# Kernel optimization log

Hardware: AMD Instinct MI355X
Metric: run time of the kernel (lower is better)

## Reference

```python
import jax, jax.numpy as jnp
import numpy as np

B, I, H = 4096, 1024, 1024

def setup_inputs() -> dict:
    key = jax.random.key(0)
    ks = jax.random.split(key, 10)
    return {
        "input": jax.random.normal(ks[0], (B, I), dtype=jnp.float32),
        "hx": jax.random.normal(ks[1], (B, H), dtype=jnp.float32),
        "cx": jax.random.normal(ks[2], (B, H), dtype=jnp.float32),
        "noise_q": jax.random.uniform(ks[3], (1,), dtype=jnp.float32),
        "noise_e": jax.random.uniform(ks[4], (1,), dtype=jnp.float32),
        "weight_ih": jax.random.normal(ks[5], (4 * H, I), dtype=jnp.float32),
        "weight_hh": jax.random.normal(ks[6], (4 * H, H), dtype=jnp.float32),
        "bias_ih": jax.random.normal(ks[7], (4 * H,), dtype=jnp.float32),
        "bias_hh": jax.random.normal(ks[8], (4 * H,), dtype=jnp.float32),
        # pre-drawn standard-normal noise (torch.randn in the original forward)
        "eps_c": jax.random.normal(jax.random.fold_in(key, 101), (B, H), dtype=jnp.float32),
        "eps_h": jax.random.normal(jax.random.fold_in(key, 102), (B, H), dtype=jnp.float32),
    }

def reference(input, hx, cx, noise_q, noise_e, weight_ih, weight_hh, bias_ih, bias_hh, eps_c, eps_h):
    # gates: [B, 4H]
    gates = input @ weight_ih.T + bias_ih + hx @ weight_hh.T + bias_hh
    ingate, forgetgate, cellgate, outgate = jnp.split(gates, 4, axis=1)
    ingate = jax.nn.sigmoid(ingate)
    forgetgate = jax.nn.sigmoid(forgetgate)
    cellgate = jnp.tanh(cellgate)
    outgate = jax.nn.sigmoid(outgate)
    cy = forgetgate * cx + ingate * cellgate + jnp.sqrt(noise_e) * eps_c
    hy = outgate * jnp.tanh(cy) + jnp.sqrt(noise_q) * eps_h
    return (hy, cy)
```

## Files before the change

kernel.cpp:

```cpp
#include <hip/hip_runtime.h>
#include <hip/hip_bf16.h>
#include <cstdint>
#include <cstddef>


#define B_ROWS 4096
#define HDIM   1024
#define KDIM   2048
#define BM     256
#define BK     32
#define T_STEPS (KDIM / BK)

typedef unsigned short u16;
using f32x4  = __attribute__((ext_vector_type(4))) float;
using short8 = __attribute__((ext_vector_type(8))) short;
using half8  = __attribute__((ext_vector_type(8))) _Float16;

__device__ __forceinline__ u16 f2h_bits(float f) {
    _Float16 h = (_Float16)f;
    return __builtin_bit_cast(u16, h);
}

__global__ void pack_kernel(const float* __restrict__ input, const float* __restrict__ hx,
                            const float* __restrict__ wih, const float* __restrict__ whh,
                            u16* __restrict__ Af, u16* __restrict__ Wf)
{
    const int PER = (B_ROWS * KDIM) / 4;
    int stride = gridDim.x * blockDim.x;
    for (int i = blockIdx.x * blockDim.x + threadIdx.x; i < 2 * PER; i += stride) {
        int isW = (i >= PER) ? 1 : 0;
        int e = i - isW * PER;
        int row = e >> 9;
        int k = (e & 511) << 2;
        const float* s0 = isW ? wih : input;
        const float* s1 = isW ? whh : hx;
        const float* src = (k < 1024) ? (s0 + (size_t)row * 1024 + k)
                                      : (s1 + (size_t)row * 1024 + (k - 1024));
        float4 v = *(const float4*)src;
        size_t doff = (size_t)row * KDIM + k;
        u16* dst = (isW ? Wf : Af) + doff;
        *(ushort4*)dst = make_ushort4(f2h_bits(v.x), f2h_bits(v.y),
                                      f2h_bits(v.z), f2h_bits(v.w));
    }
}

__device__ __forceinline__ void gload16(const void* g, void* l) {
    __builtin_amdgcn_global_load_lds((const __attribute__((address_space(1))) void*)g,
                                     (__attribute__((address_space(3))) void*)l, 16, 0, 0);
}
__device__ __forceinline__ float sigmf(float x) { return 1.0f / (1.0f + __expf(-x)); }
__device__ __forceinline__ float tanhfast(float x) { return 1.0f - 2.0f / (1.0f + __expf(2.0f * x)); }

__launch_bounds__(512, 2)
__global__ void lstm_fused(const u16* __restrict__ Afp, const u16* __restrict__ Wfp,
                           const float* __restrict__ cx, const float* __restrict__ eps_c,
                           const float* __restrict__ eps_h,
                           const float* __restrict__ bias_ih, const float* __restrict__ bias_hh,
                           const float* __restrict__ noise_q, const float* __restrict__ noise_e,
                           float* __restrict__ out)
{
    __shared__ __align__(16) u16 lA[3][4][256][8];
    __shared__ __align__(16) u16 lW[3][4][256][8];

    int bid = blockIdx.x;
    int w = (bid & 7) * 32 + (bid >> 3);
    int mi = w & 15;
    int hq = w >> 4;
    int bm0 = mi * BM;
    int h0 = hq * 64;

    int tid  = threadIdx.x;
    int lane = tid & 63;
    int wid  = tid >> 6;
    int wm   = wid >> 2;
    int wn   = wid & 3;

    int rSt = tid & 255;
    int kS  = tid >> 8;
    const u16* Asrc = Afp + (size_t)(bm0 + rSt) * KDIM;
    int wgrow = (rSt >> 6) * 1024 + h0 + (rSt & 63);
    const u16* Wsrc = Wfp + (size_t)wgrow * KDIM;

#define STG_A(sb, t_) do { \
        gload16(Asrc + (t_) * 32 + kS * 8,       &lA[sb][kS][rSt][0]);     \
        gload16(Asrc + (t_) * 32 + (kS + 2) * 8, &lA[sb][kS + 2][rSt][0]); } while (0)
#define STG_W(sb, t_) do { \
        gload16(Wsrc + (t_) * 32 + kS * 8,       &lW[sb][kS][rSt][0]);     \
        gload16(Wsrc + (t_) * 32 + (kS + 2) * 8, &lW[sb][kS + 2][rSt][0]); } while (0)

    int fk = lane >> 4, fr = lane & 15;

    f32x4 acc[8][4];
#pragma unroll
    for (int m = 0; m < 8; ++m)
#pragma unroll
        for (int g = 0; g < 4; ++g)
            acc[m][g] = (f32x4){0.f, 0.f, 0.f, 0.f};

    STG_A(0, 0); STG_W(0, 0);
    STG_A(1, 1); STG_W(1, 1);
    asm volatile("s_waitcnt vmcnt(4)");
    __builtin_amdgcn_s_barrier();

#define LD8(p) __builtin_bit_cast(half8, *(const short8*)(p))

#define PH_MFMA(mb, A0, A1, A2, A3) do { \
        __builtin_amdgcn_s_setprio(1); \
        _Pragma("unroll") \
        for (int g = 0; g < 4; ++g) { \
            acc[(mb)][g]     = __builtin_amdgcn_mfma_f32_16x16x32_f16(A0, wf[g], acc[(mb)][g], 0, 0, 0); \
            acc[(mb) + 1][g] = __builtin_amdgcn_mfma_f32_16x16x32_f16(A1, wf[g], acc[(mb) + 1][g], 0, 0, 0); \
        } \
        _Pragma("unroll") \
        for (int g = 0; g < 4; ++g) { \
            acc[(mb) + 2][g] = __builtin_amdgcn_mfma_f32_16x16x32_f16(A2, wf[g], acc[(mb) + 2][g], 0, 0, 0); \
            acc[(mb) + 3][g] = __builtin_amdgcn_mfma_f32_16x16x32_f16(A3, wf[g], acc[(mb) + 3][g], 0, 0, 0); \
        } \
        __builtin_amdgcn_s_setprio(0); \
    } while (0)

#define WAIT_LGKM() do { \
        asm volatile("s_waitcnt lgkmcnt(0)"); \
        __builtin_amdgcn_sched_barrier(0); \
    } while (0)

#pragma unroll 1
    for (int t = 0; t < T_STEPS; ++t) {
        int scur = t % 3;
        int spre = (t + 2) % 3;
        bool pre = (t < T_STEPS - 2);
        const u16* pA = &lA[scur][fk][wm * 128 + fr][0];
        const u16* pW = &lW[scur][fk][wn * 16 + fr][0];

        half8 wf[4];
        half8 a0, a1, a2, a3, b0, b1, b2, b3;

#pragma unroll
        for (int g = 0; g < 4; ++g) wf[g] = LD8(pW + g * 512);
        a0 = LD8(pA);           a1 = LD8(pA + 128);
        a2 = LD8(pA + 2 * 128); a3 = LD8(pA + 3 * 128);
        if (pre) STG_A(spre, t + 2);
        __builtin_amdgcn_s_barrier();
        WAIT_LGKM();
        PH_MFMA(0, a0, a1, a2, a3);
        __builtin_amdgcn_s_barrier();

        b0 = LD8(pA + 4 * 128); b1 = LD8(pA + 5 * 128);
        b2 = LD8(pA + 6 * 128); b3 = LD8(pA + 7 * 128);
        if (pre) STG_W(spre, t + 2);
        __builtin_amdgcn_s_barrier();
        WAIT_LGKM();
        PH_MFMA(4, b0, b1, b2, b3);
        if (pre) asm volatile("s_waitcnt vmcnt(4)");
        else     asm volatile("s_waitcnt vmcnt(0)");
        __builtin_amdgcn_s_barrier();
        __builtin_amdgcn_sched_barrier(0);
    }

    float sq_e = sqrtf(noise_e[0]);
    float sq_q = sqrtf(noise_q[0]);
    int h = h0 + wn * 16 + fr;
    float bsum[4];
#pragma unroll
    for (int g = 0; g < 4; ++g)
        bsum[g] = bias_ih[g * 1024 + h] + bias_hh[g * 1024 + h];
#pragma unroll
    for (int m = 0; m < 8; ++m) {
        int r0 = bm0 + wm * 128 + m * 16 + fk * 4;
#pragma unroll
        for (int j = 0; j < 4; ++j) {
            int r = r0 + j;
            float gi = acc[m][0][j] + bsum[0];
            float gf = acc[m][1][j] + bsum[1];
            float gc = acc[m][2][j] + bsum[2];
            float go = acc[m][3][j] + bsum[3];
            float ig = sigmf(gi), fg = sigmf(gf);
            float cg = tanhfast(gc), og = sigmf(go);
            size_t off = (size_t)r * HDIM + h;
            float cyv = fg * cx[off] + ig * cg + sq_e * eps_c[off];
            float hyv = og * tanhfast(cyv) + sq_q * eps_h[off];
            out[off] = hyv;
            out[(size_t)B_ROWS * HDIM + off] = cyv;
        }
    }
}

extern "C" void kernel_launch(void* const* d_in, const int* in_sizes, int n_in,
                              void* d_out, int out_size, void* d_ws, size_t ws_size,
                              hipStream_t stream)
{
    const float* input = (const float*)d_in[0];
    const float* hx    = (const float*)d_in[1];
    const float* cx    = (const float*)d_in[2];
    const float* nq    = (const float*)d_in[3];
    const float* ne    = (const float*)d_in[4];
    const float* wih   = (const float*)d_in[5];
    const float* whh   = (const float*)d_in[6];
    const float* bih   = (const float*)d_in[7];
    const float* bhh   = (const float*)d_in[8];
    const float* epsc  = (const float*)d_in[9];
    const float* epsh  = (const float*)d_in[10];
    float* out = (float*)d_out;

    u16* Af = (u16*)d_ws;
    u16* Wf = Af + (size_t)B_ROWS * KDIM;

    hipLaunchKernelGGL(pack_kernel, dim3(2048), dim3(256), 0, stream,
                       input, hx, wih, whh, Af, Wf);
    hipLaunchKernelGGL(lstm_fused, dim3(256), dim3(512), 0, stream,
                       Af, Wf, cx, epsc, epsh, bih, bhh, nq, ne, out);
}
```

Before: 113.4 us.

## Double the K tile and switch to double-buffered LDS pipeline

Raises BK from 32 to 64 and replaces the triple-buffered, two-tiles-ahead prefetch with a double buffer that prefetches one tile ahead, issuing all next-tile loads at the top of each iteration. Each iteration now runs twice as many MFMAs per barrier pair, which halves loop iterations and barrier overhead. The cost is a shallower prefetch, so global latency may be less hidden because the loop waits for vmcnt(0) every iteration. LDS use rises from 96KB to 128KB per block, which may affect occupancy at 2 blocks per CU.

```diff
diff --git a/kernel.cpp b/kernel.cpp
--- a/kernel.cpp
+++ b/kernel.cpp
@@ -8,7 +8,7 @@
 #define HDIM   1024
 #define KDIM   2048
 #define BM     256
-#define BK     32
+#define BK     64
 #define T_STEPS (KDIM / BK)
 
 typedef unsigned short u16;
@@ -59,8 +59,8 @@
                            const float* __restrict__ noise_q, const float* __restrict__ noise_e,
                            float* __restrict__ out)
 {
-    __shared__ __align__(16) u16 lA[3][4][256][8];
-    __shared__ __align__(16) u16 lW[3][4][256][8];
+    __shared__ __align__(16) u16 lA[2][8][256][8];
+    __shared__ __align__(16) u16 lW[2][8][256][8];
 
     int bid = blockIdx.x;
     int w = (bid & 7) * 32 + (bid >> 3);
@@ -81,14 +81,22 @@
     int wgrow = (rSt >> 6) * 1024 + h0 + (rSt & 63);
     const u16* Wsrc = Wfp + (size_t)wgrow * KDIM;
 
-#define STG_A(sb, t_) do { \
-        gload16(Asrc + (t_) * 32 + kS * 8,       &lA[sb][kS][rSt][0]);     \
-        gload16(Asrc + (t_) * 32 + (kS + 2) * 8, &lA[sb][kS + 2][rSt][0]); } while (0)
-#define STG_W(sb, t_) do { \
-        gload16(Wsrc + (t_) * 32 + kS * 8,       &lW[sb][kS][rSt][0]);     \
-        gload16(Wsrc + (t_) * 32 + (kS + 2) * 8, &lW[sb][kS + 2][rSt][0]); } while (0)
+#define STG_A(b, t_) do { \
+        _Pragma("unroll") \
+        for (int s = 0; s < 4; ++s) { \
+            int kc = kS + 2 * s; \
+            gload16(Asrc + (t_) * 64 + kc * 8, &lA[b][kc][rSt][0]); \
+        } } while (0)
+#define STG_W(b, t_) do { \
+        _Pragma("unroll") \
+        for (int s = 0; s < 4; ++s) { \
+            int kc = kS + 2 * s; \
+            gload16(Wsrc + (t_) * 64 + kc * 8, &lW[b][kc][rSt][0]); \
+        } } while (0)
 
     int fk = lane >> 4, fr = lane & 15;
+    const u16* pAbase = &lA[0][0][0][0] + fk * 2048 + (wm * 128 + fr) * 8;
+    const u16* pWbase = &lW[0][0][0][0] + fk * 2048 + (wn * 16 + fr) * 8;
 
     f32x4 acc[8][4];
 #pragma unroll
@@ -98,25 +106,22 @@
             acc[m][g] = (f32x4){0.f, 0.f, 0.f, 0.f};
 
     STG_A(0, 0); STG_W(0, 0);
-    STG_A(1, 1); STG_W(1, 1);
-    asm volatile("s_waitcnt vmcnt(4)");
+    asm volatile("s_waitcnt vmcnt(0)");
     __builtin_amdgcn_s_barrier();
 
 #define LD8(p) __builtin_bit_cast(half8, *(const short8*)(p))
 
-#define PH_MFMA(mb, A0, A1, A2, A3) do { \
-        __builtin_amdgcn_s_setprio(1); \
+#define MFMA16(mb, A0, A1, A2, A3, WF) do { \
         _Pragma("unroll") \
         for (int g = 0; g < 4; ++g) { \
-            acc[(mb)][g]     = __builtin_amdgcn_mfma_f32_16x16x32_f16(A0, wf[g], acc[(mb)][g], 0, 0, 0); \
-            acc[(mb) + 1][g] = __builtin_amdgcn_mfma_f32_16x16x32_f16(A1, wf[g], acc[(mb) + 1][g], 0, 0, 0); \
+            acc[(mb)][g]     = __builtin_amdgcn_mfma_f32_16x16x32_f16(A0, WF[g], acc[(mb)][g], 0, 0, 0); \
+            acc[(mb) + 1][g] = __builtin_amdgcn_mfma_f32_16x16x32_f16(A1, WF[g], acc[(mb) + 1][g], 0, 0, 0); \
         } \
         _Pragma("unroll") \
         for (int g = 0; g < 4; ++g) { \
-            acc[(mb) + 2][g] = __builtin_amdgcn_mfma_f32_16x16x32_f16(A2, wf[g], acc[(mb) + 2][g], 0, 0, 0); \
-            acc[(mb) + 3][g] = __builtin_amdgcn_mfma_f32_16x16x32_f16(A3, wf[g], acc[(mb) + 3][g], 0, 0, 0); \
+            acc[(mb) + 2][g] = __builtin_amdgcn_mfma_f32_16x16x32_f16(A2, WF[g], acc[(mb) + 2][g], 0, 0, 0); \
+            acc[(mb) + 3][g] = __builtin_amdgcn_mfma_f32_16x16x32_f16(A3, WF[g], acc[(mb) + 3][g], 0, 0, 0); \
         } \
-        __builtin_amdgcn_s_setprio(0); \
     } while (0)
 
 #define WAIT_LGKM() do { \
@@ -126,33 +131,43 @@
 
 #pragma unroll 1
     for (int t = 0; t < T_STEPS; ++t) {
-        int scur = t % 3;
-        int spre = (t + 2) % 3;
-        bool pre = (t < T_STEPS - 2);
-        const u16* pA = &lA[scur][fk][wm * 128 + fr][0];
-        const u16* pW = &lW[scur][fk][wn * 16 + fr][0];
-
-        half8 wf[4];
+        const int cur = t & 1;
+        const bool pre = (t < T_STEPS - 1);
+        const u16* pA = pAbase + cur * 16384;
+        const u16* pW = pWbase + cur * 16384;
+
+        half8 wf0[4], wf1[4];
         half8 a0, a1, a2, a3, b0, b1, b2, b3;
 
-#pragma unroll
-        for (int g = 0; g < 4; ++g) wf[g] = LD8(pW + g * 512);
+        if (pre) { STG_A(cur ^ 1, t + 1); STG_W(cur ^ 1, t + 1); }
+#pragma unroll
+        for (int g = 0; g < 4; ++g) {
+            wf0[g] = LD8(pW + g * 512);
+            wf1[g] = LD8(pW + 8192 + g * 512);
+        }
         a0 = LD8(pA);           a1 = LD8(pA + 128);
-        a2 = LD8(pA + 2 * 128); a3 = LD8(pA + 3 * 128);
-        if (pre) STG_A(spre, t + 2);
+        a2 = LD8(pA + 256);     a3 = LD8(pA + 384);
+        b0 = LD8(pA + 8192);        b1 = LD8(pA + 8192 + 128);
+        b2 = LD8(pA + 8192 + 256);  b3 = LD8(pA + 8192 + 384);
         __builtin_amdgcn_s_barrier();
         WAIT_LGKM();
-        PH_MFMA(0, a0, a1, a2, a3);
-        __builtin_amdgcn_s_barrier();
-
-        b0 = LD8(pA + 4 * 128); b1 = LD8(pA + 5 * 128);
-        b2 = LD8(pA + 6 * 128); b3 = LD8(pA + 7 * 128);
-        if (pre) STG_W(spre, t + 2);
+        __builtin_amdgcn_s_setprio(1);
+        MFMA16(0, a0, a1, a2, a3, wf0);
+        MFMA16(0, b0, b1, b2, b3, wf1);
+        __builtin_amdgcn_s_setprio(0);
+        __builtin_amdgcn_s_barrier();
+
+        a0 = LD8(pA + 512);         a1 = LD8(pA + 640);
+        a2 = LD8(pA + 768);         a3 = LD8(pA + 896);
+        b0 = LD8(pA + 8192 + 512);  b1 = LD8(pA + 8192 + 640);
+        b2 = LD8(pA + 8192 + 768);  b3 = LD8(pA + 8192 + 896);
         __builtin_amdgcn_s_barrier();
         WAIT_LGKM();
-        PH_MFMA(4, b0, b1, b2, b3);
-        if (pre) asm volatile("s_waitcnt vmcnt(4)");
-        else     asm volatile("s_waitcnt vmcnt(0)");
+        __builtin_amdgcn_s_setprio(1);
+        MFMA16(4, a0, a1, a2, a3, wf0);
+        MFMA16(4, b0, b1, b2, b3, wf1);
+        __builtin_amdgcn_s_setprio(0);
+        asm volatile("s_waitcnt vmcnt(0)");
         __builtin_amdgcn_s_barrier();
         __builtin_amdgcn_sched_barrier(0);
     }
```

Result: slower. 155.6 us (+37.2%).

## Load weight fragments directly from global into registers, bypassing LDS staging

Applied to the files above, without the earlier changes.

The weight operand no longer goes through shared memory. Each wave now loads its own weight fragments straight from global memory into a register double buffer, one K-step ahead, while the activation tile is still staged through a triple-buffered LDS ring. The main loop is unrolled by two so the register buffers can alternate. This removes half of the LDS footprint and the LDS write/read traffic for weights. In exchange, the waves that share a column slice now issue duplicate, strided 16-byte global loads, and weight load latency is hidden by only one step of register prefetch.

```diff
diff --git a/kernel.cpp b/kernel.cpp
--- a/kernel.cpp
+++ b/kernel.cpp
@@ -60,7 +60,6 @@
                            float* __restrict__ out)
 {
     __shared__ __align__(16) u16 lA[3][4][256][8];
-    __shared__ __align__(16) u16 lW[3][4][256][8];
 
     int bid = blockIdx.x;
     int w = (bid & 7) * 32 + (bid >> 3);
@@ -78,17 +77,17 @@
     int rSt = tid & 255;
     int kS  = tid >> 8;
     const u16* Asrc = Afp + (size_t)(bm0 + rSt) * KDIM;
-    int wgrow = (rSt >> 6) * 1024 + h0 + (rSt & 63);
-    const u16* Wsrc = Wfp + (size_t)wgrow * KDIM;
 
 #define STG_A(sb, t_) do { \
         gload16(Asrc + (t_) * 32 + kS * 8,       &lA[sb][kS][rSt][0]);     \
         gload16(Asrc + (t_) * 32 + (kS + 2) * 8, &lA[sb][kS + 2][rSt][0]); } while (0)
-#define STG_W(sb, t_) do { \
-        gload16(Wsrc + (t_) * 32 + kS * 8,       &lW[sb][kS][rSt][0]);     \
-        gload16(Wsrc + (t_) * 32 + (kS + 2) * 8, &lW[sb][kS + 2][rSt][0]); } while (0)
 
     int fk = lane >> 4, fr = lane & 15;
+
+    const u16* WregB[4];
+#pragma unroll
+    for (int g = 0; g < 4; ++g)
+        WregB[g] = Wfp + (size_t)(g * 1024 + h0 + wn * 16 + fr) * KDIM + fk * 8;
 
     f32x4 acc[8][4];
 #pragma unroll
@@ -97,64 +96,66 @@
         for (int g = 0; g < 4; ++g)
             acc[m][g] = (f32x4){0.f, 0.f, 0.f, 0.f};
 
-    STG_A(0, 0); STG_W(0, 0);
-    STG_A(1, 1); STG_W(1, 1);
-    asm volatile("s_waitcnt vmcnt(4)");
+#define LD8(p) __builtin_bit_cast(half8, *(const short8*)(p))
+
+    half8 wfA[4], wfB[4];
+#pragma unroll
+    for (int g = 0; g < 4; ++g) wfA[g] = LD8(WregB[g]);
+    STG_A(0, 0);
+    STG_A(1, 1);
+    asm volatile("s_waitcnt vmcnt(2)");
     __builtin_amdgcn_s_barrier();
 
-#define LD8(p) __builtin_bit_cast(half8, *(const short8*)(p))
-
-#define PH_MFMA(mb, A0, A1, A2, A3) do { \
-        __builtin_amdgcn_s_setprio(1); \
+#define MFMA16(mb, A0, A1, A2, A3, WF) do { \
         _Pragma("unroll") \
         for (int g = 0; g < 4; ++g) { \
-            acc[(mb)][g]     = __builtin_amdgcn_mfma_f32_16x16x32_f16(A0, wf[g], acc[(mb)][g], 0, 0, 0); \
-            acc[(mb) + 1][g] = __builtin_amdgcn_mfma_f32_16x16x32_f16(A1, wf[g], acc[(mb) + 1][g], 0, 0, 0); \
+            acc[(mb)][g]     = __builtin_amdgcn_mfma_f32_16x16x32_f16(A0, WF[g], acc[(mb)][g], 0, 0, 0); \
+            acc[(mb) + 1][g] = __builtin_amdgcn_mfma_f32_16x16x32_f16(A1, WF[g], acc[(mb) + 1][g], 0, 0, 0); \
         } \
         _Pragma("unroll") \
         for (int g = 0; g < 4; ++g) { \
-            acc[(mb) + 2][g] = __builtin_amdgcn_mfma_f32_16x16x32_f16(A2, wf[g], acc[(mb) + 2][g], 0, 0, 0); \
-            acc[(mb) + 3][g] = __builtin_amdgcn_mfma_f32_16x16x32_f16(A3, wf[g], acc[(mb) + 3][g], 0, 0, 0); \
+            acc[(mb) + 2][g] = __builtin_amdgcn_mfma_f32_16x16x32_f16(A2, WF[g], acc[(mb) + 2][g], 0, 0, 0); \
+            acc[(mb) + 3][g] = __builtin_amdgcn_mfma_f32_16x16x32_f16(A3, WF[g], acc[(mb) + 3][g], 0, 0, 0); \
         } \
-        __builtin_amdgcn_s_setprio(0); \
     } while (0)
 
-#define WAIT_LGKM() do { \
+#define STEP(t_, WFU, WFL) do { \
+        const int scur = (t_) % 3; \
+        const int spre = ((t_) + 2) % 3; \
+        const u16* pA = &lA[scur][fk][wm * 128 + fr][0]; \
+        half8 a0, a1, a2, a3, a4, a5, a6, a7; \
+         \
+        if ((t_) < T_STEPS - 1) { \
+            _Pragma("unroll") \
+            for (int g = 0; g < 4; ++g) WFL[g] = LD8(WregB[g] + ((t_) + 1) * 32); \
+        } \
+        if ((t_) < T_STEPS - 2) STG_A(spre, (t_) + 2); \
+        a0 = LD8(pA);       a1 = LD8(pA + 128); \
+        a2 = LD8(pA + 256); a3 = LD8(pA + 384); \
+        __builtin_amdgcn_s_barrier(); \
         asm volatile("s_waitcnt lgkmcnt(0)"); \
         __builtin_amdgcn_sched_barrier(0); \
+        __builtin_amdgcn_s_setprio(1); \
+        MFMA16(0, a0, a1, a2, a3, WFU); \
+        __builtin_amdgcn_s_setprio(0); \
+        __builtin_amdgcn_s_barrier(); \
+         \
+        a4 = LD8(pA + 512); a5 = LD8(pA + 640); \
+        a6 = LD8(pA + 768); a7 = LD8(pA + 896); \
+        __builtin_amdgcn_s_barrier(); \
+        asm volatile("s_waitcnt lgkmcnt(0)"); \
+        __builtin_amdgcn_sched_barrier(0); \
+        __builtin_amdgcn_s_setprio(1); \
+        MFMA16(4, a4, a5, a6, a7, WFU); \
+        __builtin_amdgcn_s_setprio(0); \
+        asm volatile("s_waitcnt vmcnt(2)");   \
+        __builtin_amdgcn_s_barrier(); \
     } while (0)
 
 #pragma unroll 1
-    for (int t = 0; t < T_STEPS; ++t) {
-        int scur = t % 3;
-        int spre = (t + 2) % 3;
-        bool pre = (t < T_STEPS - 2);
-        const u16* pA = &lA[scur][fk][wm * 128 + fr][0];
-        const u16* pW = &lW[scur][fk][wn * 16 + fr][0];
-
-        half8 wf[4];
-        half8 a0, a1, a2, a3, b0, b1, b2, b3;
-
-#pragma unroll
-        for (int g = 0; g < 4; ++g) wf[g] = LD8(pW + g * 512);
-        a0 = LD8(pA);           a1 = LD8(pA + 128);
-        a2 = LD8(pA + 2 * 128); a3 = LD8(pA + 3 * 128);
-        if (pre) STG_A(spre, t + 2);
-        __builtin_amdgcn_s_barrier();
-        WAIT_LGKM();
-        PH_MFMA(0, a0, a1, a2, a3);
-        __builtin_amdgcn_s_barrier();
-
-        b0 = LD8(pA + 4 * 128); b1 = LD8(pA + 5 * 128);
-        b2 = LD8(pA + 6 * 128); b3 = LD8(pA + 7 * 128);
-        if (pre) STG_W(spre, t + 2);
-        __builtin_amdgcn_s_barrier();
-        WAIT_LGKM();
-        PH_MFMA(4, b0, b1, b2, b3);
-        if (pre) asm volatile("s_waitcnt vmcnt(4)");
-        else     asm volatile("s_waitcnt vmcnt(0)");
-        __builtin_amdgcn_s_barrier();
-        __builtin_amdgcn_sched_barrier(0);
+    for (int tt = 0; tt < T_STEPS; tt += 2) {
+        STEP(tt,     wfA, wfB);
+        STEP(tt + 1, wfB, wfA);
     }
 
     float sq_e = sqrtf(noise_e[0]);
```

After: 168.9 us. 1.49x slower.
